# Kernel optimization log

Measured on AMD Instinct MI355X. Metric: run time of the kernel, lower is better.

## Reference

```python
import jax, jax.numpy as jnp
import numpy as np

EMBED = 1024
HEADS = 16
HEAD_DIM = EMBED // HEADS


def setup_inputs() -> dict:
    key = jax.random.key(0)
    ks = jax.random.split(key, 8)
    N, S = 4, 2048
    inp = {
        "values": jax.random.normal(ks[0], (N, S, EMBED), dtype=jnp.float32),
        "keys": jax.random.normal(ks[1], (N, S, EMBED), dtype=jnp.float32),
        "queries": jax.random.normal(ks[2], (N, S, EMBED), dtype=jnp.float32),
        # Linear weights stored as [in, out] (torch Linear applies x @ W.T; here W already transposed)
        "W_v": jax.random.normal(ks[3], (EMBED, EMBED), dtype=jnp.float32) / np.sqrt(EMBED),
        "W_k": jax.random.normal(ks[4], (EMBED, EMBED), dtype=jnp.float32) / np.sqrt(EMBED),
        "W_q": jax.random.normal(ks[5], (EMBED, EMBED), dtype=jnp.float32) / np.sqrt(EMBED),
        "W_o": jax.random.normal(ks[6], (EMBED, EMBED), dtype=jnp.float32) / np.sqrt(EMBED),
        "b_o": jax.random.normal(ks[7], (EMBED,), dtype=jnp.float32) * 0.01,
    }
    return inp


def reference(values, keys, queries, W_v, W_k, W_q, W_o, b_o):
    N, q_len, _ = queries.shape
    v = (values @ W_v).reshape(N, -1, HEADS, HEAD_DIM)   # [n, v_len, h, d]
    k = (keys @ W_k).reshape(N, -1, HEADS, HEAD_DIM)     # [n, k_len, h, d]
    q = (queries @ W_q).reshape(N, -1, HEADS, HEAD_DIM)  # [n, q_len, h, d]
    # NOTE: original scales by sqrt(embed_size), not sqrt(head_dim)
    energy = jnp.einsum('nqhd,nkhd->nhqk', q, k) / jnp.sqrt(jnp.float32(EMBED))
    attn = jax.nn.softmax(energy, axis=-1)
    out = jnp.einsum('nhqk,nkhd->nqhd', attn, v).reshape(N, q_len, EMBED)
    return out @ W_o + b_o
```

## Files before the change

kernel.cpp:

```cpp
#include <hip/hip_runtime.h>
#include <hip/hip_bf16.h>
#include <stdint.h>

typedef __attribute__((ext_vector_type(8))) short short8;
typedef __attribute__((ext_vector_type(4))) float f32x4;
typedef unsigned short u16;

#define EMBED 1024
#define SEQ 2048
#define NBATCH 4
#define MROWS (NBATCH * SEQ)

__device__ __forceinline__ u16 f2bf(float f) {
  union { float f; uint32_t u; } v; v.f = f;
  uint32_t r = v.u + 0x7fffu + ((v.u >> 16) & 1u);
  return (u16)(r >> 16);
}

__device__ __forceinline__ uint32_t cvtpk(float lo, float hi) {
  uint32_t r;
  asm("v_cvt_pk_bf16_f32 %0, %1, %2" : "=v"(r) : "v"(lo), "v"(hi));
  return r;
}

__device__ __forceinline__ float vexp2(float x) {
  float r;
  asm("v_exp_f32 %0, %1" : "=v"(r) : "v"(x));
  return r;
}

__device__ __forceinline__ void gld16(const void* g, void* l) {
  __builtin_amdgcn_global_load_lds((const __attribute__((address_space(1))) void*)g,
                                   (__attribute__((address_space(3))) void*)l, 16, 0, 0);
}

__global__ __launch_bounds__(256) void prep_kernel(const float* __restrict__ W0,
                                                   const float* __restrict__ W1,
                                                   const float* __restrict__ W2,
                                                   const float* __restrict__ W3,
                                                   u16* __restrict__ T0,
                                                   u16* __restrict__ T1,
                                                   u16* __restrict__ T2,
                                                   u16* __restrict__ T3) {
  int id = blockIdx.x;
  int z = id >> 10;
  const float* W = z == 0 ? W0 : (z == 1 ? W1 : (z == 2 ? W2 : W3));
  u16* Wt = z == 0 ? T0 : (z == 1 ? T1 : (z == 2 ? T2 : T3));
  __shared__ float tile[32][33];
  int bx = (id & 31) * 32, by = ((id >> 5) & 31) * 32;
  int tx = threadIdx.x & 31, ty = threadIdx.x >> 5;
#pragma unroll
  for (int i = 0; i < 32; i += 8)
    tile[ty + i][tx] = W[(size_t)(by + ty + i) * EMBED + bx + tx];
  __syncthreads();
#pragma unroll
  for (int i = 0; i < 32; i += 8)
    Wt[(size_t)(bx + ty + i) * EMBED + by + tx] = f2bf(tile[tx][ty + i]);
}

__global__ __launch_bounds__(256) void qkv_gemm(const float* __restrict__ Aq,
                                                const float* __restrict__ Ak,
                                                const float* __restrict__ Av,
                                                const u16* __restrict__ Wqt,
                                                const u16* __restrict__ Wkt,
                                                const u16* __restrict__ Wvt,
                                                u16* __restrict__ Qb,
                                                u16* __restrict__ Kb,
                                                u16* __restrict__ Vtb,
                                                float qscale) {
  constexpr int K = 1024;
  __shared__ float lsAf[2][128 * 32];
  __shared__ u16   lsB[2][128 * 32];

  const int id = blockIdx.x;
  const int xcd = id & 7;
  const int rest = id >> 3;
  const int bx = rest & 7;
  const int p = (rest >> 3) * 8 + xcd;
  const int z = p >> 6;
  const int by = p & 63;

  const float* A = z == 0 ? Aq : (z == 1 ? Ak : Av);
  const u16* Bt  = z == 0 ? Wqt : (z == 1 ? Wkt : Wvt);
  u16* outp      = z == 0 ? Qb : (z == 1 ? Kb : Vtb);
  const float oscale = z == 0 ? qscale : 1.0f;
  const int epi = (z == 2) ? 1 : 0;

  const int t = threadIdx.x, l = t & 63, w = t >> 6;
  const int g = l >> 4, r15 = l & 15;
  const int m0 = by * 128, n0 = bx * 128;
  const int wm = (w >> 1) * 64, wn = (w & 1) * 64;
  f32x4 acc[4][4] = {};

  const float* Apf[4];
#pragma unroll
  for (int j = 0; j < 4; ++j) {
    int row = j * 32 + (t >> 3);
    Apf[j] = A + (size_t)(m0 + row) * K + (size_t)(((t & 7) ^ (row & 7)) * 4);
  }
  const u16* Bp[2];
#pragma unroll
  for (int j = 0; j < 2; ++j) {
    int row = j * 64 + (t >> 2);
    Bp[j] = Bt + (size_t)(n0 + row) * K + (size_t)(((t & 3) ^ (row & 3)) * 8);
  }

  auto STAGE = [&](int buf, int k0) {
#pragma unroll
    for (int j = 0; j < 4; ++j)
      gld16(Apf[j] + k0, (char*)&lsAf[buf][0] + j * 4096 + t * 16);
#pragma unroll
    for (int j = 0; j < 2; ++j)
      gld16(Bp[j] + k0, (char*)&lsB[buf][0] + j * 4096 + t * 16);
  };

  auto COMPUTE = [&](int buf) {
    short8 af[4], bfv[4];
#pragma unroll
    for (int mi = 0; mi < 4; ++mi) {
      int row = wm + mi * 16 + r15;
      int s = row & 7;
      const char* base = (const char*)&lsAf[buf][0] + row * 128;
      f32x4 a0 = *(const f32x4*)(base + (((2 * g) ^ s) * 16));
      f32x4 a1 = *(const f32x4*)(base + (((2 * g + 1) ^ s) * 16));
      union { uint32_t u[4]; short8 sv; } pu;
      pu.u[0] = cvtpk(a0[0], a0[1]);
      pu.u[1] = cvtpk(a0[2], a0[3]);
      pu.u[2] = cvtpk(a1[0], a1[1]);
      pu.u[3] = cvtpk(a1[2], a1[3]);
      af[mi] = pu.sv;
    }
#pragma unroll
    for (int ni = 0; ni < 4; ++ni) {
      int row = wn + ni * 16 + r15;
      bfv[ni] = *(const short8*)((const char*)&lsB[buf][0] + row * 64 + ((g ^ (row & 3)) * 16));
    }
#pragma unroll
    for (int mi = 0; mi < 4; ++mi)
#pragma unroll
      for (int ni = 0; ni < 4; ++ni)
        acc[mi][ni] = __builtin_amdgcn_mfma_f32_16x16x32_bf16(af[mi], bfv[ni], acc[mi][ni], 0, 0, 0);
  };

  STAGE(0, 0);
  asm volatile("s_waitcnt vmcnt(0)" ::: "memory");
  __builtin_amdgcn_s_barrier();

#pragma unroll 1
  for (int it = 0; it < 16; ++it) {
    int k0 = it * 64;
    STAGE(1, k0 + 32);
    COMPUTE(0);
    asm volatile("s_waitcnt vmcnt(0)" ::: "memory");
    __builtin_amdgcn_s_barrier();
    if (it < 15) STAGE(0, k0 + 64);
    COMPUTE(1);
    if (it < 15) {
      asm volatile("s_waitcnt vmcnt(0)" ::: "memory");
      __builtin_amdgcn_s_barrier();
    }
  }

#pragma unroll
  for (int mi = 0; mi < 4; ++mi)
#pragma unroll
    for (int ni = 0; ni < 4; ++ni)
#pragma unroll
      for (int r = 0; r < 4; ++r) {
        int row = m0 + wm + mi * 16 + g * 4 + r;
        int col = n0 + wn + ni * 16 + r15;
        float v = acc[mi][ni][r];
        if (epi == 0) {
          ((u16*)outp)[(((size_t)(row >> 11) * 16 + (col >> 6)) * SEQ + (row & 2047)) * 64 + (col & 63)] = f2bf(v * oscale);
        } else {
          ((u16*)outp)[(((size_t)(row >> 11) * 16 + (col >> 6)) * 64 + (col & 63)) * SEQ + (row & 2047)] = f2bf(v);
        }
      }
}

__global__ __launch_bounds__(256) void gemm_o(const u16* __restrict__ A,
                                              const u16* __restrict__ Bt,
                                              float* __restrict__ outp,
                                              const float* __restrict__ bias) {
  constexpr int K = 1024;
  __shared__ u16 lsA[128 * 64];
  __shared__ u16 lsB[128 * 64];

  const int id = blockIdx.x;
  const int xcd = id & 7;
  const int rest = id >> 3;
  const int bx = rest & 7;
  const int by = (rest >> 3) * 8 + xcd;

  const int t = threadIdx.x, l = t & 63, w = t >> 6;
  const int g = l >> 4, r15 = l & 15;
  const int m0 = by * 128, n0 = bx * 128;
  const int wm = (w >> 1) * 64, wn = (w & 1) * 64;
  f32x4 acc[4][4] = {};
  const int srow = t >> 3;
  const int sc16 = (t & 7) * 16;

  const u16* Ap[4]; const u16* Bp[4];
#pragma unroll
  for (int j = 0; j < 4; ++j) {
    int row = srow + j * 32;
    int colswz = (sc16 ^ ((row & 7) << 4)) >> 1;
    Ap[j] = A  + (size_t)(m0 + row) * K + colswz;
    Bp[j] = Bt + (size_t)(n0 + row) * K + colswz;
  }

  for (int k0 = 0; k0 < K; k0 += 64) {
#pragma unroll
    for (int j = 0; j < 4; ++j) {
      gld16(Ap[j] + k0, lsA + j * 2048 + w * 512);
      gld16(Bp[j] + k0, lsB + j * 2048 + w * 512);
    }
    __syncthreads();
    short8 af[2][4], bfv[2][4];
#pragma unroll
    for (int kk = 0; kk < 2; ++kk) {
#pragma unroll
      for (int mi = 0; mi < 4; ++mi) {
        int row = wm + mi * 16 + r15;
        af[kk][mi] = *(const short8*)((const char*)lsA + row * 128 + ((kk * 64 + g * 16) ^ ((row & 7) << 4)));
      }
#pragma unroll
      for (int ni = 0; ni < 4; ++ni) {
        int row = wn + ni * 16 + r15;
        bfv[kk][ni] = *(const short8*)((const char*)lsB + row * 128 + ((kk * 64 + g * 16) ^ ((row & 7) << 4)));
      }
    }
#pragma unroll
    for (int kk = 0; kk < 2; ++kk)
#pragma unroll
      for (int mi = 0; mi < 4; ++mi)
#pragma unroll
        for (int ni = 0; ni < 4; ++ni)
          acc[mi][ni] = __builtin_amdgcn_mfma_f32_16x16x32_bf16(af[kk][mi], bfv[kk][ni], acc[mi][ni], 0, 0, 0);
    __syncthreads();
  }

#pragma unroll
  for (int mi = 0; mi < 4; ++mi)
#pragma unroll
    for (int ni = 0; ni < 4; ++ni)
#pragma unroll
      for (int r = 0; r < 4; ++r) {
        int row = m0 + wm + mi * 16 + g * 4 + r;
        int col = n0 + wn + ni * 16 + r15;
        outp[(size_t)row * EMBED + col] = acc[mi][ni][r] + bias[col];
      }
}

__global__ __launch_bounds__(256) void attn_kernel(const u16* __restrict__ Q,
                                                   const u16* __restrict__ Kb,
                                                   const u16* __restrict__ Vt,
                                                   u16* __restrict__ AO) {
  __shared__ u16 lsK[3][64 * 64];
  __shared__ u16 lsV[2][64 * 64];
  const int t = threadIdx.x, l = t & 63, w = t >> 6;
  const int g = l >> 4, r15 = l & 15;

  const int flat = blockIdx.x;
  const int work = (flat & 7) * 128 + (flat >> 3);
  const int bh = work >> 4;
  const int q0 = (work & 15) * 128;

  const u16* Qh = Q + (size_t)bh * SEQ * 64;
  const u16* Kh = Kb + (size_t)bh * SEQ * 64;
  const u16* Vh = Vt + (size_t)bh * 64 * SEQ;

  short8 qf[2][2];
#pragma unroll
  for (int qi = 0; qi < 2; ++qi)
#pragma unroll
    for (int dh = 0; dh < 2; ++dh)
      qf[qi][dh] = *(const short8*)&Qh[(size_t)(q0 + w * 32 + qi * 16 + r15) * 64 + dh * 32 + g * 8];

  const short8 kones = { 0x3F80, 0x3F80, 0x3F80, 0x3F80, 0x3F80, 0x3F80, 0x3F80, 0x3F80 };
  f32x4 ssum[2] = {};
  f32x4 oacc[4][2] = {};

  const int srow = t >> 3;
  const int scolb = (t & 7) * 16;

  uint4 vreg[2][2];

  auto STAGE_K = [&](int buf, int kv0) {
#pragma unroll
    for (int j = 0; j < 2; ++j) {
      int row = j * 32 + srow;
      int colswz = (scolb ^ ((row & 7) << 4)) >> 1;
      gld16(Kh + (size_t)(kv0 + row) * 64 + colswz, &lsK[buf][j * 2048 + w * 512]);
    }
  };
  auto VLOAD = [&](int par, int kv0) {
#pragma unroll
    for (int j = 0; j < 2; ++j) {
      int row = j * 32 + srow;
      vreg[par][j] = *(const uint4*)(Vh + (size_t)row * SEQ + kv0 + (scolb >> 1));
    }
  };
  auto VSTORE = [&](int buf, int par) {
#pragma unroll
    for (int j = 0; j < 2; ++j) {
      int row = j * 32 + srow;
      int c4 = (row & 7) << 4, c3 = ((row >> 3) & 1) << 3;
      char* base = (char*)&lsV[buf][0] + row * 128 + (scolb ^ c4);
      *(uint2*)(base + c3)       = make_uint2(vreg[par][j].x, vreg[par][j].y);
      *(uint2*)(base + (8 ^ c3)) = make_uint2(vreg[par][j].z, vreg[par][j].w);
    }
  };

  auto COMPUTE = [&](const u16* Kc, const u16* Vc) {
    f32x4 sacc[2][4] = {};
    __builtin_amdgcn_s_setprio(1);
#pragma unroll
    for (int c = 0; c < 4; ++c) {
      int krow = c * 16 + r15;
      int sz = (krow & 7) << 4;
#pragma unroll
      for (int dh = 0; dh < 2; ++dh) {
        short8 kf = *(const short8*)((const char*)Kc + krow * 128 + ((dh * 64 + g * 16) ^ sz));
#pragma unroll
        for (int qi = 0; qi < 2; ++qi)
          sacc[qi][c] = __builtin_amdgcn_mfma_f32_16x16x32_bf16(kf, qf[qi][dh], sacc[qi][c], 0, 0, 0);
      }
    }
    __builtin_amdgcn_s_setprio(0);

    short8 pb[2][2];
#pragma unroll
    for (int qi = 0; qi < 2; ++qi) {
#pragma unroll
      for (int c = 0; c < 4; ++c)
#pragma unroll
        for (int r = 0; r < 4; ++r)
          sacc[qi][c][r] = vexp2(sacc[qi][c][r]);
#pragma unroll
      for (int kh = 0; kh < 2; ++kh) {
        union { uint32_t u[4]; short8 s; } pu;
        pu.u[0] = cvtpk(sacc[qi][2 * kh][0],     sacc[qi][2 * kh][1]);
        pu.u[1] = cvtpk(sacc[qi][2 * kh][2],     sacc[qi][2 * kh][3]);
        pu.u[2] = cvtpk(sacc[qi][2 * kh + 1][0], sacc[qi][2 * kh + 1][1]);
        pu.u[3] = cvtpk(sacc[qi][2 * kh + 1][2], sacc[qi][2 * kh + 1][3]);
        pb[qi][kh] = pu.s;
      }
    }
#pragma unroll
    for (int qi = 0; qi < 2; ++qi)
#pragma unroll
      for (int kh = 0; kh < 2; ++kh)
        ssum[qi] = __builtin_amdgcn_mfma_f32_16x16x32_bf16(kones, pb[qi][kh], ssum[qi], 0, 0, 0);

    __builtin_amdgcn_s_setprio(1);
#pragma unroll
    for (int dc = 0; dc < 4; ++dc) {
      int vrow = dc * 16 + r15;
      int sz = ((vrow & 7) << 4) | (((vrow >> 3) & 1) << 3);
      const char* vb = (const char*)Vc + vrow * 128;
#pragma unroll
      for (int kh = 0; kh < 2; ++kh) {
        union { uint2 v[2]; short8 s; } va;
        va.v[0] = *(const uint2*)(vb + ((kh * 64 + 8 * g) ^ sz));
        va.v[1] = *(const uint2*)(vb + ((kh * 64 + 32 + 8 * g) ^ sz));
#pragma unroll
        for (int qi = 0; qi < 2; ++qi)
          oacc[dc][qi] = __builtin_amdgcn_mfma_f32_16x16x32_bf16(va.s, pb[qi][kh], oacc[dc][qi], 0, 0, 0);
      }
    }
    __builtin_amdgcn_s_setprio(0);
  };

  auto STEP = [&](int tt, int kb, int vb, bool stv, bool ld) {
    if (stv) VSTORE((tt + 1) & 1, (tt + 1) & 1);
    if (ld) {
      VLOAD(tt & 1, (tt + 2) * 64);
      STAGE_K((tt + 2) % 3, (tt + 2) * 64);
    }
    COMPUTE(lsK[kb], lsV[vb]);
    if (tt < 31) {
      if (ld) asm volatile("s_waitcnt vmcnt(4)" ::: "memory");
      else    asm volatile("s_waitcnt vmcnt(0)" ::: "memory");
      asm volatile("s_waitcnt lgkmcnt(0)" ::: "memory");
      __builtin_amdgcn_s_barrier();
      __builtin_amdgcn_sched_barrier(0);
    }
  };

  VLOAD(0, 0);        STAGE_K(0, 0);
  VLOAD(1, 64);       STAGE_K(1, 64);
  VSTORE(0, 0);
  asm volatile("s_waitcnt vmcnt(4)" ::: "memory");
  asm volatile("s_waitcnt lgkmcnt(0)" ::: "memory");
  __builtin_amdgcn_s_barrier();
  __builtin_amdgcn_sched_barrier(0);

#pragma unroll 1
  for (int it = 0; it < 5; ++it) {
    int base = it * 6;
    STEP(base + 0, 0, 0, true, true);
    STEP(base + 1, 1, 1, true, true);
    STEP(base + 2, 2, 0, true, true);
    STEP(base + 3, 0, 1, true, true);
    STEP(base + 4, 1, 0, true, true);
    STEP(base + 5, 2, 1, true, true);
  }
  STEP(30, 0, 0, true, false);
  STEP(31, 1, 1, false, false);

  const int nb = bh >> 4, h = bh & 15;
  float inv[2] = { 1.0f / ssum[0][0], 1.0f / ssum[1][0] };
#pragma unroll
  for (int dc = 0; dc < 4; ++dc)
#pragma unroll
    for (int qi = 0; qi < 2; ++qi) {
      int q = q0 + w * 32 + qi * 16 + r15;
      int d = dc * 16 + g * 4;
      uint32_t a = cvtpk(oacc[dc][qi][0] * inv[qi], oacc[dc][qi][1] * inv[qi]);
      uint32_t b = cvtpk(oacc[dc][qi][2] * inv[qi], oacc[dc][qi][3] * inv[qi]);
      uint2* dst = (uint2*)&AO[((size_t)(nb * SEQ + q)) * EMBED + h * 64 + d];
      *dst = make_uint2(a, b);
    }
}

extern "C" void kernel_launch(void* const* d_in, const int* in_sizes, int n_in,
                              void* d_out, int out_size, void* d_ws, size_t ws_size,
                              hipStream_t stream) {
  const float* values  = (const float*)d_in[0];
  const float* keys    = (const float*)d_in[1];
  const float* queries = (const float*)d_in[2];
  const float* W_v = (const float*)d_in[3];
  const float* W_k = (const float*)d_in[4];
  const float* W_q = (const float*)d_in[5];
  const float* W_o = (const float*)d_in[6];
  const float* b_o = (const float*)d_in[7];

  const size_t XSZ = (size_t)MROWS * EMBED;
  const size_t WSZ = (size_t)EMBED * EMBED;
  u16* ws = (u16*)d_ws;
  u16* Wvt = ws;
  u16* Wkt = Wvt + WSZ;
  u16* Wqt = Wkt + WSZ;
  u16* Wot = Wqt + WSZ;
  u16* Qb  = Wot + WSZ;
  u16* Kb  = Qb + XSZ;
  u16* Vtb = Kb + XSZ;
  u16* AO  = Vtb + XSZ;

  prep_kernel<<<4096, 256, 0, stream>>>(W_v, W_k, W_q, W_o, Wvt, Wkt, Wqt, Wot);

  const float QSCALE = 0.03125f * 1.4426950408889634f;
  qkv_gemm<<<1536, 256, 0, stream>>>(queries, keys, values, Wqt, Wkt, Wvt, Qb, Kb, Vtb, QSCALE);

  attn_kernel<<<1024, 256, 0, stream>>>(Qb, Kb, Vtb, AO);

  gemm_o<<<512, 256, 0, stream>>>(AO, Wot, (float*)d_out, b_o);
}
```

Measured before the change: 213.0 us.

## Triple-buffer A and stage wider B tiles with partial vmcnt waits in QKV GEMM

Restructures the QKV projection GEMM pipeline: the fp32 A tile gets three LDS buffers, and B is staged in 64-wide K chunks with a new 8-way XOR swizzle. The main loop now waits on partial vmcnt counts, so loads for future stages stay in flight while the current stage computes, instead of draining all loads before each barrier. This aims to hide global memory latency better. The cost is more LDS per block, which may lower occupancy, plus more complex buffer rotation logic.

New measurement: 225.0 us. 5.6% more time.

```diff
diff --git a/kernel.cpp b/kernel.cpp
--- a/kernel.cpp
+++ b/kernel.cpp
@@ -69,8 +69,8 @@
                                                 u16* __restrict__ Vtb,
                                                 float qscale) {
   constexpr int K = 1024;
-  __shared__ float lsAf[2][128 * 32];
-  __shared__ u16   lsB[2][128 * 32];
+  __shared__ float lsAf[3][128 * 32];
+  __shared__ u16   lsB[2][128 * 64];
 
   const int id = blockIdx.x;
   const int xcd = id & 7;
@@ -96,31 +96,34 @@
 #pragma unroll
   for (int j = 0; j < 4; ++j) {
     int row = j * 32 + (t >> 3);
-    Apf[j] = A + (size_t)(m0 + row) * K + (size_t)(((t & 7) ^ (row & 7)) * 4);
-  }
-  const u16* Bp[2];
-#pragma unroll
-  for (int j = 0; j < 2; ++j) {
-    int row = j * 64 + (t >> 2);
-    Bp[j] = Bt + (size_t)(n0 + row) * K + (size_t)(((t & 3) ^ (row & 3)) * 8);
-  }
-
-  auto STAGE = [&](int buf, int k0) {
+    Apf[j] = A + (size_t)(m0 + row) * K + ((t & 7) ^ (row & 7)) * 4;
+  }
+  const u16* Bp[4];
+#pragma unroll
+  for (int j = 0; j < 4; ++j) {
+    int row = j * 32 + (t >> 3);
+    int colswz = (((t & 7) * 16) ^ ((row & 7) << 4)) >> 1;
+    Bp[j] = Bt + (size_t)(n0 + row) * K + colswz;
+  }
+
+  auto STAGE_A = [&](int buf, int k0) {
 #pragma unroll
     for (int j = 0; j < 4; ++j)
-      gld16(Apf[j] + k0, (char*)&lsAf[buf][0] + j * 4096 + t * 16);
-#pragma unroll
-    for (int j = 0; j < 2; ++j)
-      gld16(Bp[j] + k0, (char*)&lsB[buf][0] + j * 4096 + t * 16);
-  };
-
-  auto COMPUTE = [&](int buf) {
+      gld16(Apf[j] + k0, (char*)&lsAf[buf][0] + j * 4096 + w * 1024);
+  };
+  auto STAGE_B = [&](int buf, int k0) {
+#pragma unroll
+    for (int j = 0; j < 4; ++j)
+      gld16(Bp[j] + k0, (char*)&lsB[buf][0] + j * 4096 + w * 1024);
+  };
+
+  auto COMPUTE = [&](int abuf, int bbuf, int kk) {
     short8 af[4], bfv[4];
 #pragma unroll
     for (int mi = 0; mi < 4; ++mi) {
       int row = wm + mi * 16 + r15;
       int s = row & 7;
-      const char* base = (const char*)&lsAf[buf][0] + row * 128;
+      const char* base = (const char*)&lsAf[abuf][0] + row * 128;
       f32x4 a0 = *(const f32x4*)(base + (((2 * g) ^ s) * 16));
       f32x4 a1 = *(const f32x4*)(base + (((2 * g + 1) ^ s) * 16));
       union { uint32_t u[4]; short8 sv; } pu;
@@ -133,7 +136,7 @@
 #pragma unroll
     for (int ni = 0; ni < 4; ++ni) {
       int row = wn + ni * 16 + r15;
-      bfv[ni] = *(const short8*)((const char*)&lsB[buf][0] + row * 64 + ((g ^ (row & 3)) * 16));
+      bfv[ni] = *(const short8*)((const char*)&lsB[bbuf][0] + row * 128 + ((kk * 64 + g * 16) ^ ((row & 7) << 4)));
     }
 #pragma unroll
     for (int mi = 0; mi < 4; ++mi)
@@ -142,24 +145,40 @@
         acc[mi][ni] = __builtin_amdgcn_mfma_f32_16x16x32_bf16(af[mi], bfv[ni], acc[mi][ni], 0, 0, 0);
   };
 
-  STAGE(0, 0);
-  asm volatile("s_waitcnt vmcnt(0)" ::: "memory");
+  STAGE_A(0, 0);
+  STAGE_B(0, 0);
+  STAGE_A(1, 32);
+  asm volatile("s_waitcnt vmcnt(0) lgkmcnt(0)" ::: "memory");
   __builtin_amdgcn_s_barrier();
+  __builtin_amdgcn_sched_barrier(0);
+
+  int aC = 0, aP = 1, aQ = 2;
+  int bC = 0;
 
 #pragma unroll 1
-  for (int it = 0; it < 16; ++it) {
-    int k0 = it * 64;
-    STAGE(1, k0 + 32);
-    COMPUTE(0);
-    asm volatile("s_waitcnt vmcnt(0)" ::: "memory");
+  for (int hp = 0; hp < 15; ++hp) {
+    STAGE_A(aQ, (2 * hp + 2) * 32);
+    STAGE_B(bC ^ 1, (hp + 1) * 64);
+    COMPUTE(aC, bC, 0);
+    asm volatile("s_waitcnt vmcnt(8)" ::: "memory");
+    asm volatile("s_waitcnt lgkmcnt(0)" ::: "memory");
     __builtin_amdgcn_s_barrier();
-    if (it < 15) STAGE(0, k0 + 64);
-    COMPUTE(1);
-    if (it < 15) {
-      asm volatile("s_waitcnt vmcnt(0)" ::: "memory");
-      __builtin_amdgcn_s_barrier();
-    }
-  }
+    __builtin_amdgcn_sched_barrier(0);
+    STAGE_A(aC, (2 * hp + 3) * 32);
+    COMPUTE(aP, bC, 1);
+    asm volatile("s_waitcnt vmcnt(4)" ::: "memory");
+    asm volatile("s_waitcnt lgkmcnt(0)" ::: "memory");
+    __builtin_amdgcn_s_barrier();
+    __builtin_amdgcn_sched_barrier(0);
+    int tmp = aQ; aQ = aP; aP = aC; aC = tmp;
+    bC ^= 1;
+  }
+
+  COMPUTE(aC, bC, 0);
+  asm volatile("s_waitcnt vmcnt(0) lgkmcnt(0)" ::: "memory");
+  __builtin_amdgcn_s_barrier();
+  __builtin_amdgcn_sched_barrier(0);
+  COMPUTE(aP, bC, 1);
 
 #pragma unroll
   for (int mi = 0; mi < 4; ++mi)
```
